# Kernel optimization log

Measured on AMD Instinct MI355X. Metric: run time of the kernel, lower is better.

Reference implementation:

```python
import jax, jax.numpy as jnp
import numpy as np

B, IN, OUT = 2048, 64, 2048


def setup_inputs() -> dict:
    key = jax.random.key(0)
    k1, k2, k3 = jax.random.split(key, 3)
    x = jax.random.normal(k1, (B, IN), dtype=jnp.float32)
    # learned params (shapes per init: means [in, out], inv_std_dev [out, in, in])
    means = jax.random.uniform(k2, (IN, OUT), dtype=jnp.float32)
    # roughly like the inverse of a diagonal step matrix plus small noise
    inv_std_dev = (jax.random.normal(k3, (OUT, IN, IN), dtype=jnp.float32) * 0.05
                   + jnp.eye(IN, dtype=jnp.float32) * 0.5)
    return {"x": x, "means": means, "inv_std_dev": inv_std_dev}


def reference(x, means, inv_std_dev):
    # diff[b, o, i] = x[b, i] - means[i, o]   -> [B, OUT, IN]
    d = x[:, None, :] - means.T[None, :, :]
    # torch uses inv_std_dev.pow(2) (elementwise square), not a matrix square
    A = inv_std_dev * inv_std_dev  # [OUT, IN, IN]
    # per-neuron quadratic form: q[b, o] = d[b,o,:] @ A[o] @ d[b,o,:]
    q = jnp.einsum('boi,oij,boj->bo', d, A, d)
    return jnp.exp(-0.5 * q)  # [B, OUT]
```

## Files before the change

kernel.cpp:

```cpp
#include <hip/hip_runtime.h>
#include <hip/hip_bf16.h>

typedef __bf16 bf16x8 __attribute__((ext_vector_type(8)));
typedef float f32x16 __attribute__((ext_vector_type(16)));

#define B_N 2048
#define O_N 2048
#define K_TRI 2080
#define K_TOT 2304
#define K_STEPS 36
#define CHUNKS 288

__device__ __forceinline__ void gld16(const void* g, void* l) {
    __builtin_amdgcn_global_load_lds(
        (const __attribute__((address_space(1))) void*)g,
        (__attribute__((address_space(3))) void*)l,
        16, 0, 0);
}

__global__ __launch_bounds__(256) void rbf_prep3(
    const float* __restrict__ inv, const float* __restrict__ means,
    const float* __restrict__ x, __bf16* __restrict__ St, __bf16* __restrict__ Pt)
{
    __shared__ float s[64 * 65];
    __shared__ float mld[64];
    __shared__ float uw[128];
    __shared__ unsigned short ptab[K_TRI];
    __shared__ unsigned short obuf[CHUNKS * 64];

    const int t = threadIdx.x;
    {
        int base = 0;
#pragma unroll 1
        for (int i = 0; i < 64; ++i) {
            if (t < 64 - i) ptab[base + t] = (unsigned short)((i << 8) | (i + t));
            base += 64 - i;
        }
    }
    const bool isS = (int)blockIdx.x < 256;
    const int g0 = (isS ? (int)blockIdx.x : (int)blockIdx.x - 256) * 8;

    if (isS) {
#pragma unroll 1
        for (int r8 = 0; r8 < 8; ++r8) {
            const int o = g0 + r8;
            __syncthreads();
            const float4* src = (const float4*)(inv + (size_t)o * 4096);
#pragma unroll
            for (int k = 0; k < 4; ++k) {
                const int idx = k * 256 + t;
                const float4 v = src[idx];
                const int i = idx >> 4;
                const int j0 = (idx & 15) * 4;
                s[i * 65 + j0 + 0] = v.x * v.x;
                s[i * 65 + j0 + 1] = v.y * v.y;
                s[i * 65 + j0 + 2] = v.z * v.z;
                s[i * 65 + j0 + 3] = v.w * v.w;
            }
            if (t < 64) mld[t] = means[(size_t)t * O_N + o];
            __syncthreads();
            if (t < 64) {
                float u = 0.f;
#pragma unroll
                for (int i = 0; i < 64; ++i) u = fmaf(s[i * 65 + t], mld[i], u);
                uw[t] = u;
            } else if (t < 128) {
                const int j = t - 64;
                float w = 0.f;
#pragma unroll
                for (int i = 0; i < 64; ++i) w = fmaf(s[j * 65 + i], mld[i], w);
                uw[64 + j] = w;
            }
            __syncthreads();
#pragma unroll 1
            for (int c = t; c < K_TOT; c += 256) {
                float v;
                if (c < K_TRI) {
                    const int ij = ptab[c];
                    const int i = ij >> 8, j = ij & 255;
                    v = (i == j) ? s[i * 65 + i] : (s[i * 65 + j] + s[j * 65 + i]);
                } else if (c < 2272) {
                    const int j = (c - K_TRI) & 63;
                    const float cv = -(uw[j] + uw[64 + j]);
                    const __bf16 hi = (__bf16)cv;
                    v = (c < 2208) ? (float)hi : (cv - (float)hi);
                } else if (c < 2274) {
                    float kk = 0.f;
#pragma unroll
                    for (int j = 0; j < 64; ++j) kk = fmaf(uw[j], mld[j], kk);
                    const __bf16 khi = (__bf16)kk;
                    v = (c == 2272) ? (float)khi : (kk - (float)khi);
                } else v = 0.f;
                obuf[(c >> 3) * 64 + r8 * 8 + (c & 7)] =
                    __builtin_bit_cast(unsigned short, (__bf16)v);
            }
        }
    } else {
#pragma unroll
        for (int q = 0; q < 2; ++q) {
            const int idx = q * 256 + t;
            s[(idx >> 6) * 65 + (idx & 63)] = x[(size_t)(g0 + (idx >> 6)) * 64 + (idx & 63)];
        }
        __syncthreads();
#pragma unroll 1
        for (int r8 = 0; r8 < 8; ++r8) {
            const float* xr = &s[r8 * 65];
#pragma unroll 1
            for (int c = t; c < K_TOT; c += 256) {
                float v;
                if (c < K_TRI) {
                    const int ij = ptab[c];
                    v = xr[ij >> 8] * xr[ij & 255];
                } else if (c < 2272) {
                    const float xv = xr[(c - K_TRI) & 63];
                    const __bf16 hi = (__bf16)xv;
                    v = (c < 2144) ? (float)hi
                      : (c < 2208) ? (xv - (float)hi) : (float)hi;
                } else if (c < 2274) v = 1.f;
                else v = 0.f;
                obuf[(c >> 3) * 64 + r8 * 8 + (c & 7)] =
                    __builtin_bit_cast(unsigned short, (__bf16)v);
            }
        }
    }
    __syncthreads();
    __bf16* dst = isS ? St : Pt;
#pragma unroll 1
    for (int idx = t; idx < CHUNKS * 8; idx += 256) {
        const int chunk = idx >> 3, r8 = idx & 7;
        const bf16x8 v = *(const bf16x8*)&obuf[chunk * 64 + r8 * 8];
        *(bf16x8*)(dst + ((size_t)chunk * 2048 + g0 + r8) * 8) = v;
    }
}

__global__ __launch_bounds__(256, 1) void rbf_gemm(
    const __bf16* __restrict__ P, const __bf16* __restrict__ S,
    float* __restrict__ out)
{
    __shared__ __align__(16) char sAB[4][32768];

    const int tid = threadIdx.x;
    const int lane = tid & 63;
    const int w = tid >> 6;
    const int wr = w >> 1, wc = w & 1;
    const int cl = lane & 31;
    const int h = lane >> 5;

    const int wg = (int)blockIdx.x;
    const int xcd = wg & 7;
    const int loc = wg >> 3;
    const int oBase = (xcd * 2 + (loc & 1)) * 128;
    const int bBase = (loc >> 1) * 128;

    const char* gsrc[8];
#pragma unroll
    for (int r = 0; r < 8; ++r) {
        const int ks = (r & 3) * 2 + (tid >> 7);
        const int row = tid & 127;
        gsrc[r] = (r < 4)
            ? (const char*)P + ((size_t)ks * 2048 + bBase + row) * 16
            : (const char*)S + ((size_t)ks * 2048 + oBase + row) * 16;
    }

#define RBF_STAGE(ST) do {                                                    \
    const size_t go_ = (size_t)(ST) * 262144;      \
    char* d_ = &sAB[(ST) & 3][0];                                             \
    _Pragma("unroll")                                                         \
    for (int r_ = 0; r_ < 8; ++r_)                                            \
        gld16(gsrc[r_] + go_, d_ + r_ * 4096 + tid * 16);                     \
} while (0)

    RBF_STAGE(0);
    RBF_STAGE(1);

    const f32x16 zz = {0.f,0.f,0.f,0.f,0.f,0.f,0.f,0.f,
                       0.f,0.f,0.f,0.f,0.f,0.f,0.f,0.f};
    f32x16 acc00 = zz, acc01 = zz, acc10 = zz, acc11 = zz;

    const int aoff = (wr * 64 + cl) * 16;
    const int boff = 16384 + (wc * 64 + cl) * 16;

#pragma unroll 1
    for (int st = 0; st < K_STEPS; ++st) {
        if (st + 2 < K_STEPS) {
            RBF_STAGE(st + 2);
            asm volatile("s_waitcnt vmcnt(16)" ::: "memory");
        } else if (st + 1 < K_STEPS) {
            asm volatile("s_waitcnt vmcnt(8)" ::: "memory");
        } else {
            asm volatile("s_waitcnt vmcnt(0)" ::: "memory");
        }
        __builtin_amdgcn_s_barrier();
        const char* bp = &sAB[st & 3][0];

        __builtin_amdgcn_s_setprio(1);
#pragma unroll
        for (int sl = 0; sl < 4; ++sl) {
            const int kso = (sl * 2 + h) * 2048;
            const bf16x8 a0 = *(const bf16x8*)(bp + kso + aoff);
            const bf16x8 a1 = *(const bf16x8*)(bp + kso + aoff + 512);
            const bf16x8 b0 = *(const bf16x8*)(bp + kso + boff);
            const bf16x8 b1 = *(const bf16x8*)(bp + kso + boff + 512);
            acc00 = __builtin_amdgcn_mfma_f32_32x32x16_bf16(a0, b0, acc00, 0, 0, 0);
            acc01 = __builtin_amdgcn_mfma_f32_32x32x16_bf16(a0, b1, acc01, 0, 0, 0);
            acc10 = __builtin_amdgcn_mfma_f32_32x32x16_bf16(a1, b0, acc10, 0, 0, 0);
            acc11 = __builtin_amdgcn_mfma_f32_32x32x16_bf16(a1, b1, acc11, 0, 0, 0);
        }
        __builtin_amdgcn_s_setprio(0);
    }
#undef RBF_STAGE

#pragma unroll
    for (int r = 0; r < 16; ++r) {
        const int row32 = (r & 3) + 8 * (r >> 2) + 4 * h;
        const size_t r0 = (size_t)(bBase + wr * 64 + row32) * O_N;
        const size_t r1 = (size_t)(bBase + wr * 64 + 32 + row32) * O_N;
        const int c0 = oBase + wc * 64 + cl;
        const int c1 = oBase + wc * 64 + 32 + cl;
        out[r0 + c0] = exp2f(acc00[r] * -0.72134752044448170368f);
        out[r0 + c1] = exp2f(acc01[r] * -0.72134752044448170368f);
        out[r1 + c0] = exp2f(acc10[r] * -0.72134752044448170368f);
        out[r1 + c1] = exp2f(acc11[r] * -0.72134752044448170368f);
    }
}

extern "C" void kernel_launch(void* const* d_in, const int* in_sizes, int n_in,
                              void* d_out, int out_size, void* d_ws, size_t ws_size,
                              hipStream_t stream)
{
    const float* x = (const float*)d_in[0];
    const float* means = (const float*)d_in[1];
    const float* inv = (const float*)d_in[2];
    float* out = (float*)d_out;

    __bf16* St = (__bf16*)d_ws;
    __bf16* Pt = (__bf16*)((char*)d_ws + (size_t)K_STEPS * 8 * 2048 * 16);

    rbf_prep3<<<dim3(512), dim3(256), 0, stream>>>(inv, means, x, St, Pt);
    rbf_gemm<<<dim3(256), dim3(256), 0, stream>>>(Pt, St, out);

    (void)in_sizes; (void)n_in; (void)out_size; (void)ws_size;
}
```

Baseline: 63.51 us.

## Split S prep into per-neuron blocks plus transpose kernel; halve GEMM tile for occupancy

```diff
diff --git a/kernel.cpp b/kernel.cpp
--- a/kernel.cpp
+++ b/kernel.cpp
@@ -9,7 +9,6 @@
 #define K_TRI 2080
 #define K_TOT 2304
 #define K_STEPS 36
-#define CHUNKS 288
 
 __device__ __forceinline__ void gld16(const void* g, void* l) {
     __builtin_amdgcn_global_load_lds(
@@ -18,15 +17,15 @@
         16, 0, 0);
 }
 
-__global__ __launch_bounds__(256) void rbf_prep3(
+__global__ __launch_bounds__(256) void rbf_prepA(
     const float* __restrict__ inv, const float* __restrict__ means,
-    const float* __restrict__ x, __bf16* __restrict__ St, __bf16* __restrict__ Pt)
+    const float* __restrict__ x, __bf16* __restrict__ Srm,
+    __bf16* __restrict__ Pt)
 {
     __shared__ float s[64 * 65];
     __shared__ float mld[64];
     __shared__ float uw[128];
     __shared__ unsigned short ptab[K_TRI];
-    __shared__ unsigned short obuf[CHUNKS * 64];
 
     const int t = threadIdx.x;
     {
@@ -37,76 +36,76 @@
             base += 64 - i;
         }
     }
-    const bool isS = (int)blockIdx.x < 256;
-    const int g0 = (isS ? (int)blockIdx.x : (int)blockIdx.x - 256) * 8;
-
-    if (isS) {
-#pragma unroll 1
-        for (int r8 = 0; r8 < 8; ++r8) {
-            const int o = g0 + r8;
-            __syncthreads();
-            const float4* src = (const float4*)(inv + (size_t)o * 4096);
-#pragma unroll
-            for (int k = 0; k < 4; ++k) {
-                const int idx = k * 256 + t;
-                const float4 v = src[idx];
-                const int i = idx >> 4;
-                const int j0 = (idx & 15) * 4;
-                s[i * 65 + j0 + 0] = v.x * v.x;
-                s[i * 65 + j0 + 1] = v.y * v.y;
-                s[i * 65 + j0 + 2] = v.z * v.z;
-                s[i * 65 + j0 + 3] = v.w * v.w;
-            }
-            if (t < 64) mld[t] = means[(size_t)t * O_N + o];
-            __syncthreads();
-            if (t < 64) {
-                float u = 0.f;
-#pragma unroll
-                for (int i = 0; i < 64; ++i) u = fmaf(s[i * 65 + t], mld[i], u);
-                uw[t] = u;
-            } else if (t < 128) {
-                const int j = t - 64;
-                float w = 0.f;
-#pragma unroll
-                for (int i = 0; i < 64; ++i) w = fmaf(s[j * 65 + i], mld[i], w);
-                uw[64 + j] = w;
-            }
-            __syncthreads();
-#pragma unroll 1
-            for (int c = t; c < K_TOT; c += 256) {
-                float v;
-                if (c < K_TRI) {
-                    const int ij = ptab[c];
-                    const int i = ij >> 8, j = ij & 255;
-                    v = (i == j) ? s[i * 65 + i] : (s[i * 65 + j] + s[j * 65 + i]);
-                } else if (c < 2272) {
-                    const int j = (c - K_TRI) & 63;
-                    const float cv = -(uw[j] + uw[64 + j]);
-                    const __bf16 hi = (__bf16)cv;
-                    v = (c < 2208) ? (float)hi : (cv - (float)hi);
-                } else if (c < 2274) {
-                    float kk = 0.f;
-#pragma unroll
-                    for (int j = 0; j < 64; ++j) kk = fmaf(uw[j], mld[j], kk);
-                    const __bf16 khi = (__bf16)kk;
-                    v = (c == 2272) ? (float)khi : (kk - (float)khi);
-                } else v = 0.f;
-                obuf[(c >> 3) * 64 + r8 * 8 + (c & 7)] =
-                    __builtin_bit_cast(unsigned short, (__bf16)v);
-            }
+
+    if ((int)blockIdx.x < O_N) {
+        const int o = blockIdx.x;
+        const float4* src = (const float4*)(inv + (size_t)o * 4096);
+#pragma unroll
+        for (int k = 0; k < 4; ++k) {
+            const int idx = k * 256 + t;
+            const float4 v = src[idx];
+            const int i = idx >> 4;
+            const int j0 = (idx & 15) * 4;
+            s[i * 65 + j0 + 0] = v.x * v.x;
+            s[i * 65 + j0 + 1] = v.y * v.y;
+            s[i * 65 + j0 + 2] = v.z * v.z;
+            s[i * 65 + j0 + 3] = v.w * v.w;
+        }
+        if (t < 64) mld[t] = means[(size_t)t * O_N + o];
+        __syncthreads();
+        if (t < 64) {
+            float u = 0.f;
+#pragma unroll
+            for (int i = 0; i < 64; ++i) u = fmaf(s[i * 65 + t], mld[i], u);
+            uw[t] = u;
+        } else if (t < 128) {
+            const int j = t - 64;
+            float w = 0.f;
+#pragma unroll
+            for (int i = 0; i < 64; ++i) w = fmaf(s[j * 65 + i], mld[i], w);
+            uw[64 + j] = w;
+        }
+        __syncthreads();
+        __bf16* Srow = Srm + (size_t)o * K_TOT;
+#pragma unroll 1
+        for (int c = t; c < K_TOT; c += 256) {
+            float v;
+            if (c < K_TRI) {
+                const int ij = ptab[c];
+                const int i = ij >> 8, j = ij & 255;
+                v = (i == j) ? s[i * 65 + i] : (s[i * 65 + j] + s[j * 65 + i]);
+            } else if (c < 2272) {
+                const int j = (c - K_TRI) & 63;
+                const float cv = -(uw[j] + uw[64 + j]);
+                const __bf16 hi = (__bf16)cv;
+                v = (c < 2208) ? (float)hi : (cv - (float)hi);
+            } else if (c < 2274) {
+                float kk = 0.f;
+#pragma unroll
+                for (int j = 0; j < 64; ++j) kk = fmaf(uw[j], mld[j], kk);
+                const __bf16 khi = (__bf16)kk;
+                v = (c == 2272) ? (float)khi : (kk - (float)khi);
+            } else v = 0.f;
+            Srow[c] = (__bf16)v;
         }
     } else {
+        const int b0r = ((int)blockIdx.x - O_N) * 8;
 #pragma unroll
         for (int q = 0; q < 2; ++q) {
             const int idx = q * 256 + t;
-            s[(idx >> 6) * 65 + (idx & 63)] = x[(size_t)(g0 + (idx >> 6)) * 64 + (idx & 63)];
+            s[(idx >> 6) * 65 + (idx & 63)] =
+                x[(size_t)(b0r + (idx >> 6)) * 64 + (idx & 63)];
         }
         __syncthreads();
 #pragma unroll 1
-        for (int r8 = 0; r8 < 8; ++r8) {
+        for (int q = 0; q < 9; ++q) {
+            const int task = q * 256 + t;
+            const int c8 = task >> 3, r8 = task & 7;
             const float* xr = &s[r8 * 65];
-#pragma unroll 1
-            for (int c = t; c < K_TOT; c += 256) {
+            unsigned short w8[8];
+#pragma unroll
+            for (int e = 0; e < 8; ++e) {
+                const int c = c8 * 8 + e;
                 float v;
                 if (c < K_TRI) {
                     const int ij = ptab[c];
@@ -118,26 +117,46 @@
                       : (c < 2208) ? (xv - (float)hi) : (float)hi;
                 } else if (c < 2274) v = 1.f;
                 else v = 0.f;
-                obuf[(c >> 3) * 64 + r8 * 8 + (c & 7)] =
-                    __builtin_bit_cast(unsigned short, (__bf16)v);
+                w8[e] = __builtin_bit_cast(unsigned short, (__bf16)v);
             }
-        }
+            *(bf16x8*)(Pt + ((size_t)c8 * 2048 + b0r + r8) * 8) =
+                *(const bf16x8*)w8;
+        }
+    }
+}
+
+__global__ __launch_bounds__(256, 2) void rbf_prepB(
+    const __bf16* __restrict__ Srm, __bf16* __restrict__ St)
+{
+    __shared__ __align__(16) char ts[64 * 1156];
+    const int t = threadIdx.x;
+    const int tb = (int)blockIdx.x >> 2;
+    const int cp = (int)blockIdx.x & 3;
+    const int o0 = tb * 64;
+
+#pragma unroll 1
+    for (int q = 0; q < 18; ++q) {
+        const int idx = q * 256 + t;
+        const int r = idx / 72, c = idx % 72;
+        const float4 v = *(const float4*)((const char*)Srm
+                          + (size_t)(o0 + r) * (K_TOT * 2) + cp * 1152 + c * 16);
+        *(float4*)(&ts[r * 1156 + c * 16]) = v;
     }
     __syncthreads();
-    __bf16* dst = isS ? St : Pt;
-#pragma unroll 1
-    for (int idx = t; idx < CHUNKS * 8; idx += 256) {
-        const int chunk = idx >> 3, r8 = idx & 7;
-        const bf16x8 v = *(const bf16x8*)&obuf[chunk * 64 + r8 * 8];
-        *(bf16x8*)(dst + ((size_t)chunk * 2048 + g0 + r8) * 8) = v;
-    }
-}
-
-__global__ __launch_bounds__(256, 1) void rbf_gemm(
+#pragma unroll 1
+    for (int q = 0; q < 18; ++q) {
+        const int idx = q * 256 + t;
+        const int c = idx >> 6, r = idx & 63;
+        const float4 v = *(const float4*)(&ts[r * 1156 + c * 16]);
+        *(float4*)((char*)St + ((size_t)(cp * 72 + c) * 2048 + o0 + r) * 16) = v;
+    }
+}
+
+__global__ __launch_bounds__(256, 2) void rbf_gemm(
     const __bf16* __restrict__ P, const __bf16* __restrict__ S,
     float* __restrict__ out)
 {
-    __shared__ __align__(16) char sAB[4][32768];
+    __shared__ __align__(16) char sAB[3][24576];
 
     const int tid = threadIdx.x;
     const int lane = tid & 63;
@@ -149,25 +168,34 @@
     const int wg = (int)blockIdx.x;
     const int xcd = wg & 7;
     const int loc = wg >> 3;
-    const int oBase = (xcd * 2 + (loc & 1)) * 128;
-    const int bBase = (loc >> 1) * 128;
-
-    const char* gsrc[8];
-#pragma unroll
-    for (int r = 0; r < 8; ++r) {
-        const int ks = (r & 3) * 2 + (tid >> 7);
-        const int row = tid & 127;
-        gsrc[r] = (r < 4)
-            ? (const char*)P + ((size_t)ks * 2048 + bBase + row) * 16
-            : (const char*)S + ((size_t)ks * 2048 + oBase + row) * 16;
+    const int oBase = (xcd * 4 + (loc & 3)) * 64;
+    const int bBase = (loc >> 2) * 128;
+
+    const char* gsrc[6];
+    int ldst[6];
+#pragma unroll
+    for (int r = 0; r < 6; ++r) {
+        if (r < 4) {
+            const int ks = 2 * r + (tid >> 7);
+            const int row = tid & 127;
+            ldst[r] = r * 4096 + tid * 16;
+            gsrc[r] = (const char*)P + ((size_t)ks * 2048 + bBase + row) * 16;
+        } else {
+            const int ks = (r - 4) * 4 + (tid >> 6);
+            const int row = tid & 63;
+            ldst[r] = 16384 + (r - 4) * 4096 + tid * 16;
+            gsrc[r] = (const char*)S + ((size_t)ks * 2048 + oBase + row) * 16;
+        }
     }
 
 #define RBF_STAGE(ST) do {                                                    \
-    const size_t go_ = (size_t)(ST) * 262144;      \
-    char* d_ = &sAB[(ST) & 3][0];                                             \
+    const size_t goA_ = (size_t)(ST) * 262144;       \
+    const size_t goB_ = (size_t)(ST) * 262144;    \
+    char* d_ = &sAB[(ST) % 3][0];                                             \
     _Pragma("unroll")                                                         \
-    for (int r_ = 0; r_ < 8; ++r_)                                            \
-        gld16(gsrc[r_] + go_, d_ + r_ * 4096 + tid * 16);                     \
+    for (int r_ = 0; r_ < 4; ++r_) gld16(gsrc[r_] + goA_, d_ + ldst[r_]);     \
+    _Pragma("unroll")                                                         \
+    for (int r_ = 4; r_ < 6; ++r_) gld16(gsrc[r_] + goB_, d_ + ldst[r_]);     \
 } while (0)
 
     RBF_STAGE(0);
@@ -175,36 +203,35 @@
 
     const f32x16 zz = {0.f,0.f,0.f,0.f,0.f,0.f,0.f,0.f,
                        0.f,0.f,0.f,0.f,0.f,0.f,0.f,0.f};
-    f32x16 acc00 = zz, acc01 = zz, acc10 = zz, acc11 = zz;
+    f32x16 acc0 = zz, acc1 = zz;
 
     const int aoff = (wr * 64 + cl) * 16;
-    const int boff = 16384 + (wc * 64 + cl) * 16;
+    const int boff = 16384 + (wc * 32 + cl) * 16;
 
 #pragma unroll 1
     for (int st = 0; st < K_STEPS; ++st) {
+        __builtin_amdgcn_s_barrier();
         if (st + 2 < K_STEPS) {
             RBF_STAGE(st + 2);
-            asm volatile("s_waitcnt vmcnt(16)" ::: "memory");
+            asm volatile("s_waitcnt vmcnt(12)" ::: "memory");
         } else if (st + 1 < K_STEPS) {
-            asm volatile("s_waitcnt vmcnt(8)" ::: "memory");
+            asm volatile("s_waitcnt vmcnt(6)" ::: "memory");
         } else {
             asm volatile("s_waitcnt vmcnt(0)" ::: "memory");
         }
         __builtin_amdgcn_s_barrier();
-        const char* bp = &sAB[st & 3][0];
+        __builtin_amdgcn_sched_barrier(0);
+        const char* bp = &sAB[st % 3][0];
 
         __builtin_amdgcn_s_setprio(1);
 #pragma unroll
         for (int sl = 0; sl < 4; ++sl) {
-            const int kso = (sl * 2 + h) * 2048;
-            const bf16x8 a0 = *(const bf16x8*)(bp + kso + aoff);
-            const bf16x8 a1 = *(const bf16x8*)(bp + kso + aoff + 512);
-            const bf16x8 b0 = *(const bf16x8*)(bp + kso + boff);
-            const bf16x8 b1 = *(const bf16x8*)(bp + kso + boff + 512);
-            acc00 = __builtin_amdgcn_mfma_f32_32x32x16_bf16(a0, b0, acc00, 0, 0, 0);
-            acc01 = __builtin_amdgcn_mfma_f32_32x32x16_bf16(a0, b1, acc01, 0, 0, 0);
-            acc10 = __builtin_amdgcn_mfma_f32_32x32x16_bf16(a1, b0, acc10, 0, 0, 0);
-            acc11 = __builtin_amdgcn_mfma_f32_32x32x16_bf16(a1, b1, acc11, 0, 0, 0);
+            const int ks = sl * 2 + h;
+            const bf16x8 a0 = *(const bf16x8*)(bp + ks * 2048 + aoff);
+            const bf16x8 a1 = *(const bf16x8*)(bp + ks * 2048 + aoff + 512);
+            const bf16x8 b0 = *(const bf16x8*)(bp + ks * 1024 + boff);
+            acc0 = __builtin_amdgcn_mfma_f32_32x32x16_bf16(a0, b0, acc0, 0, 0, 0);
+            acc1 = __builtin_amdgcn_mfma_f32_32x32x16_bf16(a1, b0, acc1, 0, 0, 0);
         }
         __builtin_amdgcn_s_setprio(0);
     }
@@ -213,14 +240,11 @@
 #pragma unroll
     for (int r = 0; r < 16; ++r) {
         const int row32 = (r & 3) + 8 * (r >> 2) + 4 * h;
-        const size_t r0 = (size_t)(bBase + wr * 64 + row32) * O_N;
-        const size_t r1 = (size_t)(bBase + wr * 64 + 32 + row32) * O_N;
-        const int c0 = oBase + wc * 64 + cl;
-        const int c1 = oBase + wc * 64 + 32 + cl;
-        out[r0 + c0] = exp2f(acc00[r] * -0.72134752044448170368f);
-        out[r0 + c1] = exp2f(acc01[r] * -0.72134752044448170368f);
-        out[r1 + c0] = exp2f(acc10[r] * -0.72134752044448170368f);
-        out[r1 + c1] = exp2f(acc11[r] * -0.72134752044448170368f);
+        const int col = oBase + wc * 32 + cl;
+        out[(size_t)(bBase + wr * 64 + row32) * O_N + col] =
+            exp2f(acc0[r] * -0.72134752044448170368f);
+        out[(size_t)(bBase + wr * 64 + 32 + row32) * O_N + col] =
+            exp2f(acc1[r] * -0.72134752044448170368f);
     }
 }
 
@@ -233,11 +257,14 @@
     const float* inv = (const float*)d_in[2];
     float* out = (float*)d_out;
 
-    __bf16* St = (__bf16*)d_ws;
-    __bf16* Pt = (__bf16*)((char*)d_ws + (size_t)K_STEPS * 8 * 2048 * 16);
-
-    rbf_prep3<<<dim3(512), dim3(256), 0, stream>>>(inv, means, x, St, Pt);
-    rbf_gemm<<<dim3(256), dim3(256), 0, stream>>>(Pt, St, out);
+    const size_t SZ = (size_t)O_N * K_TOT * sizeof(__bf16);
+    __bf16* St  = (__bf16*)d_ws;
+    __bf16* Pt  = (__bf16*)((char*)d_ws + SZ);
+    __bf16* Srm = (__bf16*)((char*)d_ws + 2 * SZ);
+
+    rbf_prepA<<<dim3(O_N + 256), dim3(256), 0, stream>>>(inv, means, x, Srm, Pt);
+    rbf_prepB<<<dim3(128), dim3(256), 0, stream>>>(Srm, St);
+    rbf_gemm<<<dim3(512), dim3(256), 0, stream>>>(Pt, St, out);
 
     (void)in_sizes; (void)n_in; (void)out_size; (void)ws_size;
 }
```

After: 65.69 us. +3.4%, slower.
